# Optimization experiments

Measured on AMD Instinct MI355X. Metric: run time of the kernel, lower is better.

Reference implementation:

```python
import math
import jax, jax.numpy as jnp
import numpy as np

B, T, C, H, DQK, DV = 2, 2048, 1024, 16, 64, 64


def setup_inputs() -> dict:
    key = jax.random.key(0)
    ks = jax.random.split(key, 5)
    x = jax.random.normal(ks[0], (B, T, C), dtype=jnp.float32)
    # randw: randn(*d) / sqrt(d[-1])
    w_q = jax.random.normal(ks[1], (H, DQK, C), dtype=jnp.float32) / math.sqrt(C)
    w_k = jax.random.normal(ks[2], (H, DQK, C), dtype=jnp.float32) / math.sqrt(C)
    w_v = jax.random.normal(ks[3], (H, DV, C), dtype=jnp.float32) / math.sqrt(C)
    w_o = jax.random.normal(ks[4], (DV * H, C), dtype=jnp.float32) / math.sqrt(C)
    return {"x": x, "w_q": w_q, "w_k": w_k, "w_v": w_v, "w_o": w_o}


def reference(x, w_q, w_k, w_v, w_o):
    # Full-sequence causal forward (bs_q.first == 0, nb == T): caches are
    # fully written in one shot, so they reduce to the plain projections.
    n, t, c = x.shape
    q = jnp.einsum('ntc,hdc->nhtd', x, w_q)
    k = jnp.einsum('ntc,hdc->nhtd', x, w_k)
    v = jnp.einsum('ntc,hdc->nhtd', x, w_v)
    scale = 1.0 / math.sqrt(w_q.shape[1])
    a = jnp.einsum('nhtd,nhsd->nhts', q, k) * scale  # [n,h,t,s]
    causal = jnp.arange(t)[:, None] < jnp.arange(t)[None, :]  # True above diag
    a = jnp.where(causal[None, None, :, :], -jnp.inf, a)
    a = jax.nn.softmax(a, axis=3)
    y = jnp.einsum('nhts,nhsd->nthd', a, v).reshape(n, t, -1)  # [n,t,h*dv]
    return y @ w_o  # cache_y, [n,t,c]
```

## Files before the change

kernel.cpp:

```cpp
#include <hip/hip_runtime.h>


typedef short bf16x4 __attribute__((ext_vector_type(4)));
typedef short bf16x8 __attribute__((ext_vector_type(8)));
typedef float f32x4 __attribute__((ext_vector_type(4)));

#define MFMA_BF16 __builtin_amdgcn_mfma_f32_16x16x32_bf16

#define QSCALE 0.18033688011112042f

__device__ __forceinline__ unsigned short f2bf(float f) {
    union { float f; unsigned u; } un; un.f = f;
    unsigned r = un.u + 0x7fffu + ((un.u >> 16) & 1u);
    return (unsigned short)(r >> 16);
}
__device__ __forceinline__ unsigned pk2(float a, float b) {
    return (unsigned)f2bf(a) | ((unsigned)f2bf(b) << 16);
}
__device__ __forceinline__ unsigned pk2t(float a, float b) {
    union { float f; unsigned u; } ua, ub; ua.f = a; ub.f = b;
    return (ua.u >> 16) | (ub.u & 0xffff0000u);
}
__device__ __forceinline__ void gload16(const void* g, void* l) {
    __builtin_amdgcn_global_load_lds(
        (const __attribute__((address_space(1))) unsigned int*)g,
        (__attribute__((address_space(3))) unsigned int*)l, 16, 0, 0);
}

__global__ __launch_bounds__(256) void prep(
    const float* __restrict__ x, const float* __restrict__ wq,
    const float* __restrict__ wk, const float* __restrict__ wv,
    const float* __restrict__ wo,
    unsigned short* __restrict__ x16, unsigned short* __restrict__ wq16,
    unsigned short* __restrict__ wk16, unsigned short* __restrict__ wv16,
    unsigned short* __restrict__ wot)
{
    const int bid = blockIdx.x;
    if (bid < 3584) {
        const float* s; unsigned short* d; int off;
        if (bid < 2048)      { s = x;  d = x16;  off = bid * 2048; }
        else if (bid < 2560) { s = wq; d = wq16; off = (bid - 2048) * 2048; }
        else if (bid < 3072) { s = wk; d = wk16; off = (bid - 2560) * 2048; }
        else                 { s = wv; d = wv16; off = (bid - 3072) * 2048; }
        int i = off + threadIdx.x * 8;
        float4 f0 = *(const float4*)&s[i], f1 = *(const float4*)&s[i + 4];
        uint4 o;
        o.x = pk2(f0.x, f0.y); o.y = pk2(f0.z, f0.w);
        o.z = pk2(f1.x, f1.y); o.w = pk2(f1.z, f1.w);
        *(uint4*)&d[i] = o;
    } else {
        __shared__ unsigned short t[64 * 72];
        const int b2 = bid - 3584;
        const int k0 = (b2 & 15) << 6, n0 = (b2 >> 4) << 6;
        const int r = threadIdx.x >> 2, cg = (threadIdx.x & 3) << 4;
        const float* src = &wo[(k0 + r) * 1024 + n0 + cg];
        #pragma unroll
        for (int j = 0; j < 16; j += 4) {
            float4 f = *(const float4*)&src[j];
            t[(cg + j + 0) * 72 + r] = f2bf(f.x);
            t[(cg + j + 1) * 72 + r] = f2bf(f.y);
            t[(cg + j + 2) * 72 + r] = f2bf(f.z);
            t[(cg + j + 3) * 72 + r] = f2bf(f.w);
        }
        __syncthreads();
        unsigned short* dst = &wot[(n0 + r) * 1024 + k0 + cg];
        unsigned short* tr = &t[r * 72 + cg];
        unsigned v[16];
        #pragma unroll
        for (int j = 0; j < 16; ++j) v[j] = tr[j];
        uint4 o0, o1;
        o0.x = v[0] | (v[1] << 16);   o0.y = v[2] | (v[3] << 16);
        o0.z = v[4] | (v[5] << 16);   o0.w = v[6] | (v[7] << 16);
        o1.x = v[8] | (v[9] << 16);   o1.y = v[10] | (v[11] << 16);
        o1.z = v[12] | (v[13] << 16); o1.w = v[14] | (v[15] << 16);
        *(uint4*)&dst[0] = o0;
        *(uint4*)&dst[8] = o1;
    }
}

__device__ __forceinline__ void gemm_body(
    const unsigned short* __restrict__ A, const unsigned short* __restrict__ Bm,
    void* __restrict__ C, int m0, int n0, int mode, int ldc, float sc)
{
    __shared__ unsigned short sa[128 * 64];
    __shared__ unsigned short sb[128 * 64];
    const int tid = threadIdx.x, wave = tid >> 6, lane = tid & 63;
    const int l15 = lane & 15, l4 = lane >> 4;
    const int wm = (wave >> 1) << 6, wn = (wave & 1) << 6;
    const int lrow = lane >> 3, lcb = (lane & 7) << 3;

    f32x4 acc[4][4] = {};

    for (int k0 = 0; k0 < 1024; k0 += 64) {
        #pragma unroll
        for (int i = 0; i < 4; ++i) {
            int rbase = i * 32 + wave * 8;
            gload16(&A[(size_t)(m0 + rbase + lrow) * 1024 + k0 + lcb], &sa[rbase * 64]);
            gload16(&Bm[(size_t)(n0 + rbase + lrow) * 1024 + k0 + lcb], &sb[rbase * 64]);
        }
        __syncthreads();
        #pragma unroll
        for (int ks = 0; ks < 2; ++ks) {
            bf16x8 af[4], bf[4];
            #pragma unroll
            for (int i = 0; i < 4; ++i)
                af[i] = *(const bf16x8*)&sa[(wm + i * 16 + l15) * 64 + ks * 32 + l4 * 8];
            #pragma unroll
            for (int j = 0; j < 4; ++j)
                bf[j] = *(const bf16x8*)&sb[(wn + j * 16 + l15) * 64 + ks * 32 + l4 * 8];
            #pragma unroll
            for (int i = 0; i < 4; ++i)
                #pragma unroll
                for (int j = 0; j < 4; ++j)
                    acc[i][j] = MFMA_BF16(af[i], bf[j], acc[i][j], 0, 0, 0);
        }
        __syncthreads();
    }

    #pragma unroll
    for (int i = 0; i < 4; ++i)
        #pragma unroll
        for (int j = 0; j < 4; ++j)
            #pragma unroll
            for (int r = 0; r < 4; ++r) {
                int row = m0 + wm + i * 16 + l4 * 4 + r;
                int col = n0 + wn + j * 16 + l15;
                float val = acc[i][j][r];
                if (mode == 0) {
                    int nb = row >> 11, t = row & 2047;
                    int hh = col >> 6, dd = col & 63;
                    ((unsigned short*)C)[(((nb << 4) + hh) * 2048 + t) * 64 + dd] =
                        f2bf(val * sc);
                } else if (mode == 1) {
                    ((float*)C)[(size_t)row * ldc + col] = val;
                } else {
                    ((unsigned short*)C)[(size_t)row * ldc + col] = f2bf(val);
                }
            }
}

__global__ __launch_bounds__(256) void proj(
    const unsigned short* __restrict__ x16,
    const unsigned short* __restrict__ wq16,
    const unsigned short* __restrict__ wk16,
    const unsigned short* __restrict__ wv16,
    unsigned short* __restrict__ qbuf,
    unsigned short* __restrict__ kbuf,
    unsigned short* __restrict__ vtb)
{
    const int bid = blockIdx.x;
    if (bid < 512) {
        int m0 = (bid & 31) << 7;
        int n0g = (bid >> 5) << 7;
        if (n0g < 1024)
            gemm_body(x16, wq16, qbuf, m0, n0g, 0, 0, QSCALE);
        else
            gemm_body(x16, wk16, kbuf, m0, n0g - 1024, 0, 0, 1.0f);
    } else {
        int v = bid - 512;
        gemm_body(wv16, x16, vtb, (v & 7) << 7, (v >> 3) << 7, 2, 4096, 1.0f);
    }
}

__global__ __launch_bounds__(256) void outp(
    const unsigned short* __restrict__ ybuf,
    const unsigned short* __restrict__ wot,
    float* __restrict__ out)
{
    __shared__ unsigned short sa[64 * 64];
    __shared__ unsigned short sb[64 * 64];
    const int tid = threadIdx.x, wave = tid >> 6, lane = tid & 63;
    const int l15 = lane & 15, l4 = lane >> 4;
    const int bid = blockIdx.x;
    const int m0 = (bid & 63) << 6, n0 = (bid >> 6) << 6;
    const int lrow = lane >> 3, lcb = (lane & 7) << 3;

    f32x4 acc[4] = {};

    for (int k0 = 0; k0 < 1024; k0 += 64) {
        #pragma unroll
        for (int i = 0; i < 2; ++i) {
            int rbase = i * 32 + wave * 8;
            gload16(&ybuf[(size_t)(m0 + rbase + lrow) * 1024 + k0 + lcb], &sa[rbase * 64]);
            gload16(&wot[(size_t)(n0 + rbase + lrow) * 1024 + k0 + lcb], &sb[rbase * 64]);
        }
        __syncthreads();
        #pragma unroll
        for (int ks = 0; ks < 2; ++ks) {
            bf16x8 af = *(const bf16x8*)&sa[(wave * 16 + l15) * 64 + ks * 32 + l4 * 8];
            #pragma unroll
            for (int j = 0; j < 4; ++j) {
                bf16x8 bf = *(const bf16x8*)&sb[(j * 16 + l15) * 64 + ks * 32 + l4 * 8];
                acc[j] = MFMA_BF16(af, bf, acc[j], 0, 0, 0);
            }
        }
        __syncthreads();
    }

    #pragma unroll
    for (int j = 0; j < 4; ++j)
        #pragma unroll
        for (int r = 0; r < 4; ++r) {
            int row = m0 + wave * 16 + l4 * 4 + r;
            int col = n0 + j * 16 + l15;
            out[(size_t)row * 1024 + col] = acc[j][r];
        }
}

__global__ __launch_bounds__(256) void attn(
    const unsigned short* __restrict__ q,
    const unsigned short* __restrict__ k,
    const unsigned short* __restrict__ vt,
    unsigned short* __restrict__ y)
{
    constexpr int P = 72;
    __shared__ unsigned short sk[2][64 * P];
    __shared__ unsigned short sv[2][64 * P];
    const int tid = threadIdx.x, wave = tid >> 6, lane = tid & 63;
    const int l15 = lane & 15, l4 = lane >> 4;
    const int bid = blockIdx.x;
    const int qtt = (bid < 512) ? (31 - (bid >> 5)) : ((bid - 512) >> 5);
    const int bh = bid & 31;
    const int nb = bh >> 4, hh = bh & 15;
    const int q0 = qtt << 6;
    const size_t base = (size_t)bh << 17;

    const int r0 = tid >> 3, c0 = (tid & 7) << 3;
    const unsigned short* kg = &k[base + ((size_t)r0 << 6) + c0];
    const unsigned short* vg = &vt[(size_t)((hh << 6) + r0) * 4096 + (nb << 11) + c0];
    const int lk0 = r0 * P + c0, lk1 = (r0 + 32) * P + c0;

    bf16x8 qf[2];
    #pragma unroll
    for (int ks = 0; ks < 2; ++ks)
        qf[ks] = *(const bf16x8*)
            &q[base + (size_t)(q0 + wave * 16 + l15) * 64 + ks * 32 + l4 * 8];

    float l_sum = 0.f;
    f32x4 acc[4] = {};

    const int nst = qtt + 1;

    {
        uint4 ka = *(const uint4*)(kg);
        uint4 kb = *(const uint4*)(kg + (32 << 6));
        uint4 va = *(const uint4*)(vg);
        uint4 vb = *(const uint4*)(vg + 32 * 4096);
        *(uint4*)&sk[0][lk0] = ka;  *(uint4*)&sk[0][lk1] = kb;
        *(uint4*)&sv[0][lk0] = va;  *(uint4*)&sv[0][lk1] = vb;
    }
    __syncthreads();

    for (int st = 0; st < nst; ++st) {
        const int cur = st & 1;
        const bool more = (st + 1) < nst;
        uint4 ka, kb, va, vb;
        if (more) {
            const int s1 = (st + 1) << 6;
            ka = *(const uint4*)(kg + ((size_t)s1 << 6));
            kb = *(const uint4*)(kg + ((size_t)(s1 + 32) << 6));
            va = *(const uint4*)(vg + s1);
            vb = *(const uint4*)(vg + 32 * 4096 + s1);
        }

        f32x4 s_acc[4] = {};
        #pragma unroll
        for (int ks = 0; ks < 2; ++ks)
            #pragma unroll
            for (int ns = 0; ns < 4; ++ns) {
                bf16x8 kf = *(const bf16x8*)&sk[cur][(ns * 16 + l15) * P + ks * 32 + l4 * 8];
                s_acc[ns] = MFMA_BF16(kf, qf[ks], s_acc[ns], 0, 0, 0);
            }

        if (st == qtt) {
            const int ql = wave * 16 + l15;
            #pragma unroll
            for (int ns = 0; ns < 4; ++ns) {
                #pragma unroll
                for (int r = 0; r < 4; ++r)
                    if (ns * 16 + l4 * 4 + r > ql) s_acc[ns][r] = -1e30f;
            }
        }

        float pe[4][4];
        #pragma unroll
        for (int ns = 0; ns < 4; ++ns) {
            #pragma unroll
            for (int r = 0; r < 4; ++r) pe[ns][r] = exp2f(s_acc[ns][r]);
            l_sum += (pe[ns][0] + pe[ns][1]) + (pe[ns][2] + pe[ns][3]);
        }

        #pragma unroll
        for (int ks = 0; ks < 2; ++ks) {
            uint4 pw;
            pw.x = pk2t(pe[2 * ks][0], pe[2 * ks][1]);
            pw.y = pk2t(pe[2 * ks][2], pe[2 * ks][3]);
            pw.z = pk2t(pe[2 * ks + 1][0], pe[2 * ks + 1][1]);
            pw.w = pk2t(pe[2 * ks + 1][2], pe[2 * ks + 1][3]);
            bf16x8 pf = *(bf16x8*)&pw;
            #pragma unroll
            for (int ds = 0; ds < 4; ++ds) {
                const unsigned short* vrow =
                    &sv[cur][(ds * 16 + l15) * P + ks * 32 + l4 * 4];
                bf16x4 lo = *(const bf16x4*)vrow;
                bf16x4 hi = *(const bf16x4*)(vrow + 16);
                bf16x8 vf = __builtin_shufflevector(lo, hi, 0, 1, 2, 3, 4, 5, 6, 7);
                acc[ds] = MFMA_BF16(vf, pf, acc[ds], 0, 0, 0);
            }
        }

        if (more) {
            const int nxt = 1 - cur;
            *(uint4*)&sk[nxt][lk0] = ka;  *(uint4*)&sk[nxt][lk1] = kb;
            *(uint4*)&sv[nxt][lk0] = va;  *(uint4*)&sv[nxt][lk1] = vb;
        }
        __syncthreads();
    }

    l_sum += __shfl_xor(l_sum, 16);
    l_sum += __shfl_xor(l_sum, 32);
    const float rl = __builtin_amdgcn_rcpf(l_sum);

    const size_t rowbase =
        ((size_t)((nb << 11) + q0 + wave * 16 + l15) << 10) + (hh << 6) + l4 * 4;
    #pragma unroll
    for (int ds = 0; ds < 4; ++ds) {
        uint2 o;
        o.x = pk2(acc[ds][0] * rl, acc[ds][1] * rl);
        o.y = pk2(acc[ds][2] * rl, acc[ds][3] * rl);
        *(uint2*)&y[rowbase + ds * 16] = o;
    }
}

extern "C" void kernel_launch(void* const* d_in, const int* in_sizes, int n_in,
                              void* d_out, int out_size, void* d_ws, size_t ws_size,
                              hipStream_t stream) {
    const float* x  = (const float*)d_in[0];
    const float* wq = (const float*)d_in[1];
    const float* wk = (const float*)d_in[2];
    const float* wv = (const float*)d_in[3];
    const float* wo = (const float*)d_in[4];
    float* out = (float*)d_out;

    const size_t M1 = 1u << 20;
    unsigned short* x16  = (unsigned short*)d_ws;
    unsigned short* wq16 = x16 + 4 * M1;
    unsigned short* wk16 = wq16 + M1;
    unsigned short* wv16 = wk16 + M1;
    unsigned short* wot  = wv16 + M1;
    unsigned short* qbuf = wot + M1;
    unsigned short* kbuf = qbuf + 4 * M1;
    unsigned short* vtb  = kbuf + 4 * M1;
    unsigned short* ybuf = vtb + 4 * M1;

    dim3 blk(256);
    prep<<<3840, blk, 0, stream>>>(x, wq, wk, wv, wo, x16, wq16, wk16, wv16, wot);
    proj<<<768, blk, 0, stream>>>(x16, wq16, wk16, wv16, qbuf, kbuf, vtb);
    attn<<<1024, blk, 0, stream>>>(qbuf, kbuf, vtb, ybuf);
    outp<<<1024, blk, 0, stream>>>(ybuf, wot, out);
}
```

Before: 193.1 us.

## Prefetch next K-tile into registers to overlap global loads with MFMA

Replaces the direct global-to-LDS loads in the projection GEMM and the output GEMM with register-staged prefetching. The next K-tile is loaded into registers while MFMAs run on the current LDS tile, then written to LDS after a barrier. The aim is to hide global memory latency, which the earlier load-then-sync-then-compute order exposed on every iteration. The cost is extra VGPRs for staging, an extra LDS write pass, and two barriers per iteration instead of one.

```diff
diff --git a/kernel.cpp b/kernel.cpp
--- a/kernel.cpp
+++ b/kernel.cpp
@@ -20,11 +20,6 @@
 __device__ __forceinline__ unsigned pk2t(float a, float b) {
     union { float f; unsigned u; } ua, ub; ua.f = a; ub.f = b;
     return (ua.u >> 16) | (ub.u & 0xffff0000u);
-}
-__device__ __forceinline__ void gload16(const void* g, void* l) {
-    __builtin_amdgcn_global_load_lds(
-        (const __attribute__((address_space(1))) unsigned int*)g,
-        (__attribute__((address_space(3))) unsigned int*)l, 16, 0, 0);
 }
 
 __global__ __launch_bounds__(256) void prep(
@@ -87,18 +82,36 @@
     const int tid = threadIdx.x, wave = tid >> 6, lane = tid & 63;
     const int l15 = lane & 15, l4 = lane >> 4;
     const int wm = (wave >> 1) << 6, wn = (wave & 1) << 6;
-    const int lrow = lane >> 3, lcb = (lane & 7) << 3;
+    const int srow = wave * 8 + (lane >> 3);
+    const int scol = (lane & 7) << 3;
+
+    const unsigned short* Ab = &A[(size_t)(m0 + srow) * 1024 + scol];
+    const unsigned short* Bb = &Bm[(size_t)(n0 + srow) * 1024 + scol];
+
+    uint4 pa[4], pb[4];
+    #pragma unroll
+    for (int i = 0; i < 4; ++i) {
+        pa[i] = *(const uint4*)(Ab + (size_t)(i * 32) * 1024);
+        pb[i] = *(const uint4*)(Bb + (size_t)(i * 32) * 1024);
+    }
+    #pragma unroll
+    for (int i = 0; i < 4; ++i) {
+        *(uint4*)&sa[(i * 32 + srow) * 64 + scol] = pa[i];
+        *(uint4*)&sb[(i * 32 + srow) * 64 + scol] = pb[i];
+    }
+    __syncthreads();
 
     f32x4 acc[4][4] = {};
 
     for (int k0 = 0; k0 < 1024; k0 += 64) {
-        #pragma unroll
-        for (int i = 0; i < 4; ++i) {
-            int rbase = i * 32 + wave * 8;
-            gload16(&A[(size_t)(m0 + rbase + lrow) * 1024 + k0 + lcb], &sa[rbase * 64]);
-            gload16(&Bm[(size_t)(n0 + rbase + lrow) * 1024 + k0 + lcb], &sb[rbase * 64]);
-        }
-        __syncthreads();
+        const bool more = (k0 + 64) < 1024;
+        if (more) {
+            #pragma unroll
+            for (int i = 0; i < 4; ++i) {
+                pa[i] = *(const uint4*)(Ab + (size_t)(i * 32) * 1024 + k0 + 64);
+                pb[i] = *(const uint4*)(Bb + (size_t)(i * 32) * 1024 + k0 + 64);
+            }
+        }
         #pragma unroll
         for (int ks = 0; ks < 2; ++ks) {
             bf16x8 af[4], bf[4];
@@ -113,6 +126,14 @@
                 #pragma unroll
                 for (int j = 0; j < 4; ++j)
                     acc[i][j] = MFMA_BF16(af[i], bf[j], acc[i][j], 0, 0, 0);
+        }
+        __syncthreads();
+        if (more) {
+            #pragma unroll
+            for (int i = 0; i < 4; ++i) {
+                *(uint4*)&sa[(i * 32 + srow) * 64 + scol] = pa[i];
+                *(uint4*)&sb[(i * 32 + srow) * 64 + scol] = pb[i];
+            }
         }
         __syncthreads();
     }
@@ -173,18 +194,36 @@
     const int l15 = lane & 15, l4 = lane >> 4;
     const int bid = blockIdx.x;
     const int m0 = (bid & 63) << 6, n0 = (bid >> 6) << 6;
-    const int lrow = lane >> 3, lcb = (lane & 7) << 3;
+    const int srow = wave * 8 + (lane >> 3);
+    const int scol = (lane & 7) << 3;
+
+    const unsigned short* Ab = &ybuf[(size_t)(m0 + srow) * 1024 + scol];
+    const unsigned short* Bb = &wot[(size_t)(n0 + srow) * 1024 + scol];
+
+    uint4 pa[2], pb[2];
+    #pragma unroll
+    for (int i = 0; i < 2; ++i) {
+        pa[i] = *(const uint4*)(Ab + (size_t)(i * 32) * 1024);
+        pb[i] = *(const uint4*)(Bb + (size_t)(i * 32) * 1024);
+    }
+    #pragma unroll
+    for (int i = 0; i < 2; ++i) {
+        *(uint4*)&sa[(i * 32 + srow) * 64 + scol] = pa[i];
+        *(uint4*)&sb[(i * 32 + srow) * 64 + scol] = pb[i];
+    }
+    __syncthreads();
 
     f32x4 acc[4] = {};
 
     for (int k0 = 0; k0 < 1024; k0 += 64) {
-        #pragma unroll
-        for (int i = 0; i < 2; ++i) {
-            int rbase = i * 32 + wave * 8;
-            gload16(&ybuf[(size_t)(m0 + rbase + lrow) * 1024 + k0 + lcb], &sa[rbase * 64]);
-            gload16(&wot[(size_t)(n0 + rbase + lrow) * 1024 + k0 + lcb], &sb[rbase * 64]);
-        }
-        __syncthreads();
+        const bool more = (k0 + 64) < 1024;
+        if (more) {
+            #pragma unroll
+            for (int i = 0; i < 2; ++i) {
+                pa[i] = *(const uint4*)(Ab + (size_t)(i * 32) * 1024 + k0 + 64);
+                pb[i] = *(const uint4*)(Bb + (size_t)(i * 32) * 1024 + k0 + 64);
+            }
+        }
         #pragma unroll
         for (int ks = 0; ks < 2; ++ks) {
             bf16x8 af = *(const bf16x8*)&sa[(wave * 16 + l15) * 64 + ks * 32 + l4 * 8];
@@ -192,6 +231,14 @@
             for (int j = 0; j < 4; ++j) {
                 bf16x8 bf = *(const bf16x8*)&sb[(j * 16 + l15) * 64 + ks * 32 + l4 * 8];
                 acc[j] = MFMA_BF16(af, bf, acc[j], 0, 0, 0);
+            }
+        }
+        __syncthreads();
+        if (more) {
+            #pragma unroll
+            for (int i = 0; i < 2; ++i) {
+                *(uint4*)&sa[(i * 32 + srow) * 64 + scol] = pa[i];
+                *(uint4*)&sb[(i * 32 + srow) * 64 + scol] = pb[i];
             }
         }
         __syncthreads();
```

Result: slower. 304.5 us (+57.7%).

## Double-buffer LDS tiles in projection and output GEMMs with K-step 32

Applied to the files above, without the earlier changes.

Both GEMM kernels (the QKV projection body and the output projection) now use two LDS buffers of K-width 32 in place of one buffer of K-width 64. The next K-slice is prefetched with global_load_lds while MFMAs run on the current slice. The goal is to hide global-load latency behind compute instead of stalling on a barrier after each load. The cost is twice as many barrier-separated iterations. The overlap may also be limited if the barrier forces a wait for all outstanding loads.

```diff
diff --git a/kernel.cpp b/kernel.cpp
--- a/kernel.cpp
+++ b/kernel.cpp
@@ -82,38 +82,51 @@
     const unsigned short* __restrict__ A, const unsigned short* __restrict__ Bm,
     void* __restrict__ C, int m0, int n0, int mode, int ldc, float sc)
 {
-    __shared__ unsigned short sa[128 * 64];
-    __shared__ unsigned short sb[128 * 64];
+    __shared__ unsigned short sa[2][128 * 32];
+    __shared__ unsigned short sb[2][128 * 32];
     const int tid = threadIdx.x, wave = tid >> 6, lane = tid & 63;
     const int l15 = lane & 15, l4 = lane >> 4;
     const int wm = (wave >> 1) << 6, wn = (wave & 1) << 6;
-    const int lrow = lane >> 3, lcb = (lane & 7) << 3;
+
+    const int r16 = lane >> 2;
+    const int gcol = (lane & 3) << 3;
+    const unsigned short* Ag0 = &A[(size_t)(m0 + wave * 16 + r16) * 1024 + gcol];
+    const unsigned short* Ag1 = Ag0 + (size_t)64 * 1024;
+    const unsigned short* Bg0 = &Bm[(size_t)(n0 + wave * 16 + r16) * 1024 + gcol];
+    const unsigned short* Bg1 = Bg0 + (size_t)64 * 1024;
+    const int lb0 = (wave * 16) * 32;
+    const int lb1 = (64 + wave * 16) * 32;
+
+    gload16(Ag0, &sa[0][lb0]);
+    gload16(Ag1, &sa[0][lb1]);
+    gload16(Bg0, &sb[0][lb0]);
+    gload16(Bg1, &sb[0][lb1]);
+    __syncthreads();
 
     f32x4 acc[4][4] = {};
 
-    for (int k0 = 0; k0 < 1024; k0 += 64) {
-        #pragma unroll
-        for (int i = 0; i < 4; ++i) {
-            int rbase = i * 32 + wave * 8;
-            gload16(&A[(size_t)(m0 + rbase + lrow) * 1024 + k0 + lcb], &sa[rbase * 64]);
-            gload16(&Bm[(size_t)(n0 + rbase + lrow) * 1024 + k0 + lcb], &sb[rbase * 64]);
-        }
-        __syncthreads();
-        #pragma unroll
-        for (int ks = 0; ks < 2; ++ks) {
-            bf16x8 af[4], bf[4];
-            #pragma unroll
-            for (int i = 0; i < 4; ++i)
-                af[i] = *(const bf16x8*)&sa[(wm + i * 16 + l15) * 64 + ks * 32 + l4 * 8];
+    for (int kk = 0; kk < 32; ++kk) {
+        const int cur = kk & 1;
+        if (kk < 31) {
+            const int off = (kk + 1) * 32;
+            const int nxt = 1 - cur;
+            gload16(Ag0 + off, &sa[nxt][lb0]);
+            gload16(Ag1 + off, &sa[nxt][lb1]);
+            gload16(Bg0 + off, &sb[nxt][lb0]);
+            gload16(Bg1 + off, &sb[nxt][lb1]);
+        }
+        bf16x8 af[4], bf4[4];
+        #pragma unroll
+        for (int i = 0; i < 4; ++i)
+            af[i] = *(const bf16x8*)&sa[cur][(wm + i * 16 + l15) * 32 + l4 * 8];
+        #pragma unroll
+        for (int j = 0; j < 4; ++j)
+            bf4[j] = *(const bf16x8*)&sb[cur][(wn + j * 16 + l15) * 32 + l4 * 8];
+        #pragma unroll
+        for (int i = 0; i < 4; ++i)
             #pragma unroll
             for (int j = 0; j < 4; ++j)
-                bf[j] = *(const bf16x8*)&sb[(wn + j * 16 + l15) * 64 + ks * 32 + l4 * 8];
-            #pragma unroll
-            for (int i = 0; i < 4; ++i)
-                #pragma unroll
-                for (int j = 0; j < 4; ++j)
-                    acc[i][j] = MFMA_BF16(af[i], bf[j], acc[i][j], 0, 0, 0);
-        }
+                acc[i][j] = MFMA_BF16(af[i], bf4[j], acc[i][j], 0, 0, 0);
         __syncthreads();
     }
 
@@ -167,32 +180,37 @@
     const unsigned short* __restrict__ wot,
     float* __restrict__ out)
 {
-    __shared__ unsigned short sa[64 * 64];
-    __shared__ unsigned short sb[64 * 64];
+    __shared__ unsigned short sa[2][64 * 32];
+    __shared__ unsigned short sb[2][64 * 32];
     const int tid = threadIdx.x, wave = tid >> 6, lane = tid & 63;
     const int l15 = lane & 15, l4 = lane >> 4;
     const int bid = blockIdx.x;
     const int m0 = (bid & 63) << 6, n0 = (bid >> 6) << 6;
-    const int lrow = lane >> 3, lcb = (lane & 7) << 3;
+
+    const int r16 = lane >> 2;
+    const int gcol = (lane & 3) << 3;
+    const unsigned short* Ag = &ybuf[(size_t)(m0 + wave * 16 + r16) * 1024 + gcol];
+    const unsigned short* Bg = &wot[(size_t)(n0 + wave * 16 + r16) * 1024 + gcol];
+    const int lb = (wave * 16) * 32;
+
+    gload16(Ag, &sa[0][lb]);
+    gload16(Bg, &sb[0][lb]);
+    __syncthreads();
 
     f32x4 acc[4] = {};
 
-    for (int k0 = 0; k0 < 1024; k0 += 64) {
-        #pragma unroll
-        for (int i = 0; i < 2; ++i) {
-            int rbase = i * 32 + wave * 8;
-            gload16(&ybuf[(size_t)(m0 + rbase + lrow) * 1024 + k0 + lcb], &sa[rbase * 64]);
-            gload16(&wot[(size_t)(n0 + rbase + lrow) * 1024 + k0 + lcb], &sb[rbase * 64]);
-        }
-        __syncthreads();
-        #pragma unroll
-        for (int ks = 0; ks < 2; ++ks) {
-            bf16x8 af = *(const bf16x8*)&sa[(wave * 16 + l15) * 64 + ks * 32 + l4 * 8];
-            #pragma unroll
-            for (int j = 0; j < 4; ++j) {
-                bf16x8 bf = *(const bf16x8*)&sb[(j * 16 + l15) * 64 + ks * 32 + l4 * 8];
-                acc[j] = MFMA_BF16(af, bf, acc[j], 0, 0, 0);
-            }
+    for (int kk = 0; kk < 32; ++kk) {
+        const int cur = kk & 1;
+        if (kk < 31) {
+            const int off = (kk + 1) * 32;
+            gload16(Ag + off, &sa[1 - cur][lb]);
+            gload16(Bg + off, &sb[1 - cur][lb]);
+        }
+        bf16x8 af = *(const bf16x8*)&sa[cur][(wave * 16 + l15) * 32 + l4 * 8];
+        #pragma unroll
+        for (int j = 0; j < 4; ++j) {
+            bf16x8 bf = *(const bf16x8*)&sb[cur][(j * 16 + l15) * 32 + l4 * 8];
+            acc[j] = MFMA_BF16(af, bf, acc[j], 0, 0, 0);
         }
         __syncthreads();
     }
```

New measurement: 184.6 us. 1.05x faster.
